# Performance work log

Measured on AMD Instinct MI355X. Metric: run time of the kernel, lower is better.

The kernel has to match this reference:

```python
import jax, jax.numpy as jnp
import numpy as np

N_HEADS = 8
EMBED_DIM = 64  # per-head dim


def setup_inputs() -> dict:
    key = jax.random.key(0)
    k1, k2, k3 = jax.random.split(key, 3)
    B, S, F = 2, 2048, 512
    x = jax.random.normal(k1, (B, S, F), dtype=jnp.float32)
    W = jax.random.normal(k2, (F, EMBED_DIM * N_HEADS * 3), dtype=jnp.float32) * 0.02
    b = jax.random.normal(k3, (EMBED_DIM * N_HEADS * 3,), dtype=jnp.float32) * 0.02
    return {"x": x, "W": W, "b": b}


def reference(x, W, b):
    B, S, F = x.shape
    H, E = N_HEADS, EMBED_DIM
    emb = x @ W + b                                   # (B, S, E*H*3)
    heads = emb.reshape(B, S, E, H, 3)
    heads = jnp.transpose(heads, (0, 4, 3, 1, 2))     # (B, 3, H, S, E)
    q, k, v = heads[:, 0], heads[:, 1], heads[:, 2]   # each (B, H, S, E)
    qk = jnp.einsum('bhse,bhte->bhst', q, k)          # (B, H, S, S)
    # Original multiplies softmax by `scaling` then divides by it -> exact cancel.
    # Note: no scaling applied BEFORE softmax in the source (faithful).
    attn = jax.nn.softmax(qk, axis=-1)
    out = jnp.einsum('bhst,bhte->bhse', attn, v)      # (B, H, S, E)
    out = jnp.transpose(out, (0, 2, 1, 3)).reshape(B, S, H * E)
    return out
```

## Files before the change

kernel.cpp:

```cpp
#include <hip/hip_runtime.h>


using half4v = __attribute__((ext_vector_type(4))) _Float16;
using half8  = __attribute__((ext_vector_type(8))) _Float16;
using f32x4  = __attribute__((ext_vector_type(4))) float;
using float4v = __attribute__((ext_vector_type(4))) float;
using uint2v = __attribute__((ext_vector_type(2))) unsigned int;
using uint4v = __attribute__((ext_vector_type(4))) unsigned int;

constexpr int BN = 2, HN = 8, SN = 2048, EN = 64, FN = 512;
constexpr size_t T_ELEMS = (size_t)BN * HN * SN * EN;

constexpr size_t WD_BYTES = (size_t)1536 * 512 * 2;
constexpr size_t BPN_OFF  = WD_BYTES;
constexpr size_t X16_OFF  = BPN_OFF + 1536 * 4;
constexpr size_t X16_BYTES = (size_t)4096 * 512 * 2;
constexpr size_t VT_OFF   = X16_OFF + X16_BYTES;
constexpr size_t VT_BYTES = T_ELEMS * 2;
constexpr size_t QKV_OFF  = VT_OFF + VT_BYTES;

__device__ inline unsigned int pack2h(float a, float b) {
  auto h = __builtin_amdgcn_cvt_pkrtz(a, b);
  return __builtin_bit_cast(unsigned int, h);
}

__device__ __forceinline__ void async_copy16(void* lds, const void* g) {
  __builtin_amdgcn_global_load_lds(
      (const __attribute__((address_space(1))) unsigned int*)g,
      (__attribute__((address_space(3))) unsigned int*)lds, 16, 0, 0);
}

__global__ __launch_bounds__(256) void prep_kernel(
    const float* __restrict__ x, const float* __restrict__ W,
    const float* __restrict__ bias, _Float16* __restrict__ x16,
    _Float16* __restrict__ Wd, float* __restrict__ bpn) {
  int t = blockIdx.x * 256 + threadIdx.x;
  const float4v* src = (const float4v*)(x + (size_t)t * 8);
  float4v a = src[0], b = src[1];
  half8 o;
  #pragma unroll
  for (int i = 0; i < 4; ++i) { o[i] = (_Float16)a[i]; o[4 + i] = (_Float16)b[i]; }
  *(half8*)(x16 + (size_t)t * 8) = o;

  if (t < 1536 * 64) {
    int n = t >> 6, cc = t & 63, fb = cc * 8;
    int ch = n >> 6, e = n & 63, c = ch >> 3, h = ch & 7;
    int j = e * 24 + h * 3 + c;
    half8 w;
    #pragma unroll
    for (int i = 0; i < 8; ++i) w[i] = (_Float16)W[(size_t)(fb + i) * 1536 + j];
    *(half8*)(Wd + (size_t)n * 512 + fb) = w;
  }
  if (t < 1536) {
    int ch = t >> 6, e = t & 63, c = ch >> 3, h = ch & 7;
    bpn[t] = bias[e * 24 + h * 3 + c];
  }
}

__global__ __launch_bounds__(256, 2) void proj_kernel(
    const _Float16* __restrict__ x16, const _Float16* __restrict__ Wd,
    const float* __restrict__ bpn, _Float16* __restrict__ qkv,
    _Float16* __restrict__ vt) {
  __shared__ __align__(16) char smem[65536];

  int tid = threadIdx.x;
  int wave = tid >> 6, lane = tid & 63;
  int q16 = lane & 15, g = lane >> 4;
  int wm = wave >> 1, wn = wave & 1;
  int gm_blk = blockIdx.x * 128, gn_blk = blockIdx.y * 128;

  f32x4 acc[4][4] = {};

  auto stage = [&](int c, int ks) {
    char* Ab = smem + c * 16384;
    char* Bb = smem + 32768 + c * 16384;
    int k0 = ks * 64;
    #pragma unroll
    for (int ii = 0; ii < 4; ++ii) {
      int qq = tid + 256 * ii;
      int row = qq >> 3, cc = qq & 7;
      int sc = (cc ^ (row & 7)) * 8;
      async_copy16(Ab + qq * 16, x16 + (size_t)(gm_blk + row) * 512 + k0 + sc);
      async_copy16(Bb + qq * 16, Wd + (size_t)(gn_blk + row) * 512 + k0 + sc);
    }
  };

  auto compute = [&](int c) {
    const char* Ab = smem + c * 16384;
    const char* Bb = smem + 32768 + c * 16384;
    #pragma unroll
    for (int kh = 0; kh < 2; ++kh) {
      half8 af[4], bf[4];
      #pragma unroll
      for (int mt = 0; mt < 4; ++mt) {
        int m = wm * 64 + mt * 16 + q16;
        af[mt] = *(const half8*)(Ab + m * 128 + ((kh * 64 + g * 16) ^ ((m & 7) << 4)));
      }
      #pragma unroll
      for (int nt = 0; nt < 4; ++nt) {
        int n = wn * 64 + nt * 16 + q16;
        bf[nt] = *(const half8*)(Bb + n * 128 + ((kh * 64 + g * 16) ^ ((n & 7) << 4)));
      }
      __builtin_amdgcn_s_setprio(1);
      #pragma unroll
      for (int mt = 0; mt < 4; ++mt)
        #pragma unroll
        for (int nt = 0; nt < 4; ++nt)
          acc[mt][nt] = __builtin_amdgcn_mfma_f32_16x16x32_f16(af[mt], bf[nt], acc[mt][nt], 0, 0, 0);
      __builtin_amdgcn_s_setprio(0);
    }
  };

  stage(0, 0);
  #pragma unroll
  for (int ks = 0; ks < 8; ++ks) {
    int cur = ks & 1;
    __syncthreads();
    if (ks + 1 < 8) {
      stage(cur ^ 1, ks + 1);
      asm volatile("s_waitcnt vmcnt(8)" ::: "memory");
    } else {
      asm volatile("s_waitcnt vmcnt(0)" ::: "memory");
    }
    __syncthreads();
    compute(cur);
  }

  int gn0 = gn_blk + wn * 64;
  int ch = gn0 >> 6, c = ch >> 3, h = ch & 7;
  int gm0 = gm_blk + wm * 64;
  if (c < 2) {
    _Float16* dst = qkv + (size_t)c * T_ELEMS;
    #pragma unroll
    for (int nt = 0; nt < 4; ++nt) {
      int e = nt * 16 + q16;
      float bv = bpn[gn0 + nt * 16 + q16];
      #pragma unroll
      for (int mt = 0; mt < 4; ++mt)
        #pragma unroll
        for (int r = 0; r < 4; ++r) {
          int gm = gm0 + mt * 16 + g * 4 + r;
          int b = gm >> 11, s = gm & 2047;
          dst[((size_t)(b * HN + h) * SN + s) * EN + e] = (_Float16)(acc[mt][nt][r] + bv);
        }
    }
  } else {
    #pragma unroll
    for (int nt = 0; nt < 4; ++nt) {
      int e = nt * 16 + q16;
      float bv = bpn[gn0 + nt * 16 + q16];
      #pragma unroll
      for (int mt = 0; mt < 4; ++mt) {
        int gm = gm0 + mt * 16 + g * 4;
        int b = gm >> 11, s = gm & 2047;
        half4v hv;
        #pragma unroll
        for (int r = 0; r < 4; ++r) hv[r] = (_Float16)(acc[mt][nt][r] + bv);
        *(half4v*)(vt + ((size_t)(b * HN + h) * EN + e) * SN + s) = hv;
      }
    }
  }
}

__global__ __launch_bounds__(256, 2) void attn_kernel(
    const _Float16* __restrict__ q_ws, const _Float16* __restrict__ k_ws,
    const _Float16* __restrict__ vt_ws, float* __restrict__ out) {
  __shared__ __align__(16) char smem[57344];

  int bid = blockIdx.x;
  int lb = (bid & 7) * 64 + (bid >> 3);
  int bh = lb >> 5, qblk = lb & 31;
  int wave = threadIdx.x >> 6, lane = threadIdx.x & 63;
  int q = lane & 15, g = lane >> 4;
  int q0 = qblk * 64 + wave * 16;

  const _Float16* qb  = q_ws  + ((size_t)bh * SN + q0) * EN;
  const _Float16* kb  = k_ws  + (size_t)bh * SN * EN;
  const _Float16* vtb = vt_ws + (size_t)bh * EN * SN;

  half8 qf[2];
  qf[0] = *(const half8*)(qb + (size_t)q * EN + g * 8);
  qf[1] = *(const half8*)(qb + (size_t)q * EN + 32 + g * 8);

  f32x4 o[4] = {};
  float m = -3e38f, l = 0.f;
  unsigned int* pw = (unsigned int*)(smem + 49152 + wave * 2048);

  int sub = lane >> 3;
  int off8 = ((lane & 7) ^ sub) * 8;
  int lin = lane * 16;

  auto stage = [&](int c, int t) {
    char* kbuf = smem + c * 16384;
    char* vbuf = kbuf + 8192;
    int kv = t * 64;
    #pragma unroll
    for (int ii = 0; ii < 2; ++ii) {
      int i = wave * 2 + ii;
      int row = i * 8 + sub;
      async_copy16(kbuf + i * 1024 + lin, kb + (size_t)(kv + row) * EN + off8);
      async_copy16(vbuf + i * 1024 + lin, vtb + (size_t)row * SN + kv + off8);
    }
  };

  int qx = (q & 7) << 4;

  auto compute = [&](int c) {
    const char* kbuf = smem + c * 16384;
    const char* vbuf = kbuf + 8192;
    half8 kf[4][2], vf[4][2];
    #pragma unroll
    for (int kt = 0; kt < 4; ++kt)
      #pragma unroll
      for (int eh = 0; eh < 2; ++eh)
        kf[kt][eh] = *(const half8*)(kbuf + ((((kt * 16 + q) * 128) + eh * 64 + g * 16) ^ qx));
    #pragma unroll
    for (int et = 0; et < 4; ++et)
      #pragma unroll
      for (int kh = 0; kh < 2; ++kh)
        vf[et][kh] = *(const half8*)(vbuf + ((((et * 16 + q) * 128) + kh * 64 + g * 16) ^ qx));

    f32x4 s[4];
    f32x4 z = {};
    __builtin_amdgcn_s_setprio(1);
    #pragma unroll
    for (int kt = 0; kt < 4; ++kt) {
      s[kt] = __builtin_amdgcn_mfma_f32_16x16x32_f16(kf[kt][0], qf[0], z, 0, 0, 0);
      s[kt] = __builtin_amdgcn_mfma_f32_16x16x32_f16(kf[kt][1], qf[1], s[kt], 0, 0, 0);
    }
    __builtin_amdgcn_s_setprio(0);

    float mx = s[0][0];
    #pragma unroll
    for (int kt = 0; kt < 4; ++kt)
      #pragma unroll
      for (int r = 0; r < 4; ++r) mx = fmaxf(mx, s[kt][r]);
    mx = fmaxf(mx, __shfl_xor(mx, 16));
    mx = fmaxf(mx, __shfl_xor(mx, 32));
    if (!__all(mx <= m + 8.f)) {
      float mn = fmaxf(m, mx);
      float scl = __expf(m - mn);
      m = mn;
      l *= scl;
      #pragma unroll
      for (int et = 0; et < 4; ++et)
        #pragma unroll
        for (int r = 0; r < 4; ++r) o[et][r] *= scl;
    }
    float ps = 0.f;
    #pragma unroll
    for (int kt = 0; kt < 4; ++kt) {
      float p0 = __expf(s[kt][0] - m), p1 = __expf(s[kt][1] - m);
      float p2 = __expf(s[kt][2] - m), p3 = __expf(s[kt][3] - m);
      ps += (p0 + p1) + (p2 + p3);
      uint2v wv;
      wv.x = pack2h(p0, p1);
      wv.y = pack2h(p2, p3);
      int w = kt * 8 + 2 * g;
      int phys = (((w >> 2) + q) & 7) * 4 + (w & 3);
      *(uint2v*)&pw[q * 32 + phys] = wv;
    }
    l += ps;
    asm volatile("s_waitcnt lgkmcnt(0)" ::: "memory");
    __builtin_amdgcn_sched_barrier(0);
    half8 pf[2];
    #pragma unroll
    for (int kh = 0; kh < 2; ++kh) {
      int cc = kh * 4 + g;
      uint4v tv = *(const uint4v*)&pw[q * 32 + ((cc + q) & 7) * 4];
      pf[kh] = __builtin_bit_cast(half8, tv);
    }
    __builtin_amdgcn_sched_barrier(0);
    __builtin_amdgcn_s_setprio(1);
    #pragma unroll
    for (int et = 0; et < 4; ++et) {
      o[et] = __builtin_amdgcn_mfma_f32_16x16x32_f16(vf[et][0], pf[0], o[et], 0, 0, 0);
      o[et] = __builtin_amdgcn_mfma_f32_16x16x32_f16(vf[et][1], pf[1], o[et], 0, 0, 0);
    }
    __builtin_amdgcn_s_setprio(0);
  };

  stage(0, 0);
  stage(1, 1);
  for (int t = 0; t < 31; ++t) {
    asm volatile("s_waitcnt vmcnt(4)" ::: "memory");
    __syncthreads();
    if (t + 2 < 32) stage((t + 2) % 3, t + 2);
    compute(t % 3);
  }
  asm volatile("s_waitcnt vmcnt(0)" ::: "memory");
  __syncthreads();
  compute(31 % 3);

  l += __shfl_xor(l, 16);
  l += __shfl_xor(l, 32);
  float rl = 1.f / l;
  int b = bh >> 3, h = bh & 7;
  float* ow = (float*)(smem + wave * 4096);
  #pragma unroll
  for (int et = 0; et < 4; ++et)
    #pragma unroll
    for (int r = 0; r < 4; ++r) {
      int e = et * 16 + g * 4 + r;
      ow[q * 64 + ((e + q * 4) & 63)] = o[et][r] * rl;
    }
  asm volatile("s_waitcnt lgkmcnt(0)" ::: "memory");
  __builtin_amdgcn_sched_barrier(0);
  #pragma unroll
  for (int qr = 0; qr < 16; ++qr) {
    float vvv = ow[qr * 64 + ((lane + qr * 4) & 63)];
    out[((size_t)b * SN + q0 + qr) * 512 + h * 64 + lane] = vvv;
  }
}

extern "C" void kernel_launch(void* const* d_in, const int* in_sizes, int n_in,
                              void* d_out, int out_size, void* d_ws, size_t ws_size,
                              hipStream_t stream) {
  const float* x    = (const float*)d_in[0];
  const float* W    = (const float*)d_in[1];
  const float* bias = (const float*)d_in[2];
  float* out = (float*)d_out;
  char* ws = (char*)d_ws;
  _Float16* Wd  = (_Float16*)(ws);
  float*    bpn = (float*)(ws + BPN_OFF);
  _Float16* x16 = (_Float16*)(ws + X16_OFF);
  _Float16* vt  = (_Float16*)(ws + VT_OFF);
  _Float16* qkv = (_Float16*)(ws + QKV_OFF);

  prep_kernel<<<1024, 256, 0, stream>>>(x, W, bias, x16, Wd, bpn);
  proj_kernel<<<dim3(32, 12), 256, 0, stream>>>(x16, Wd, bpn, qkv, vt);
  attn_kernel<<<512, 256, 0, stream>>>(qkv, qkv + T_ELEMS, vt, out);
}
```

Before: 120.1 us.

## Software-pipeline QK and PV across tiles, use exp2 with prescaled Q, shuffle P

Splits the attention inner step into a QK MFMA stage and a softmax+PV stage, then interleaves them so that the QK of tile t+1 is issued before the PV of tile t. Q is prescaled by log2(e) in the projection epilogue, so the softmax can use exp2f, and the rescale threshold is raised accordingly. The P matrix is now redistributed between lanes with cross-lane shuffles instead of an LDS round trip, which frees the per-wave P scratch area in shared memory. In exchange the kernel carries two score tile sets in registers, waits for all outstanding loads (vmcnt(0)) each step, and issues many shuffles, which may raise register pressure and stall the loads.

```diff
diff --git a/kernel.cpp b/kernel.cpp
--- a/kernel.cpp
+++ b/kernel.cpp
@@ -5,11 +5,11 @@
 using half8  = __attribute__((ext_vector_type(8))) _Float16;
 using f32x4  = __attribute__((ext_vector_type(4))) float;
 using float4v = __attribute__((ext_vector_type(4))) float;
-using uint2v = __attribute__((ext_vector_type(2))) unsigned int;
 using uint4v = __attribute__((ext_vector_type(4))) unsigned int;
 
 constexpr int BN = 2, HN = 8, SN = 2048, EN = 64, FN = 512;
 constexpr size_t T_ELEMS = (size_t)BN * HN * SN * EN;
+constexpr float LOG2E = 1.4426950408889634f;
 
 constexpr size_t WD_BYTES = (size_t)1536 * 512 * 2;
 constexpr size_t BPN_OFF  = WD_BYTES;
@@ -130,6 +130,7 @@
   int ch = gn0 >> 6, c = ch >> 3, h = ch & 7;
   int gm0 = gm_blk + wm * 64;
   if (c < 2) {
+    float qscale = (c == 0) ? LOG2E : 1.f;
     _Float16* dst = qkv + (size_t)c * T_ELEMS;
     #pragma unroll
     for (int nt = 0; nt < 4; ++nt) {
@@ -141,7 +142,7 @@
         for (int r = 0; r < 4; ++r) {
           int gm = gm0 + mt * 16 + g * 4 + r;
           int b = gm >> 11, s = gm & 2047;
-          dst[((size_t)(b * HN + h) * SN + s) * EN + e] = (_Float16)(acc[mt][nt][r] + bv);
+          dst[((size_t)(b * HN + h) * SN + s) * EN + e] = (_Float16)((acc[mt][nt][r] + bv) * qscale);
         }
     }
   } else {
@@ -165,7 +166,7 @@
 __global__ __launch_bounds__(256, 2) void attn_kernel(
     const _Float16* __restrict__ q_ws, const _Float16* __restrict__ k_ws,
     const _Float16* __restrict__ vt_ws, float* __restrict__ out) {
-  __shared__ __align__(16) char smem[57344];
+  __shared__ __align__(16) char smem[49152];
 
   int bid = blockIdx.x;
   int lb = (bid & 7) * 64 + (bid >> 3);
@@ -184,7 +185,6 @@
 
   f32x4 o[4] = {};
   float m = -3e38f, l = 0.f;
-  unsigned int* pw = (unsigned int*)(smem + 49152 + wave * 2048);
 
   int sub = lane >> 3;
   int off8 = ((lane & 7) ^ sub) * 8;
@@ -204,23 +204,18 @@
   };
 
   int qx = (q & 7) << 4;
-
-  auto compute = [&](int c) {
+  int srcA = q + 32 * (g & 1);
+  int srcB = srcA + 16;
+  bool hi = (g >> 1) != 0;
+
+  auto qk_tile = [&](int c, f32x4 (&s)[4]) {
     const char* kbuf = smem + c * 16384;
-    const char* vbuf = kbuf + 8192;
-    half8 kf[4][2], vf[4][2];
+    half8 kf[4][2];
     #pragma unroll
     for (int kt = 0; kt < 4; ++kt)
       #pragma unroll
       for (int eh = 0; eh < 2; ++eh)
         kf[kt][eh] = *(const half8*)(kbuf + ((((kt * 16 + q) * 128) + eh * 64 + g * 16) ^ qx));
-    #pragma unroll
-    for (int et = 0; et < 4; ++et)
-      #pragma unroll
-      for (int kh = 0; kh < 2; ++kh)
-        vf[et][kh] = *(const half8*)(vbuf + ((((et * 16 + q) * 128) + kh * 64 + g * 16) ^ qx));
-
-    f32x4 s[4];
     f32x4 z = {};
     __builtin_amdgcn_s_setprio(1);
     #pragma unroll
@@ -229,6 +224,16 @@
       s[kt] = __builtin_amdgcn_mfma_f32_16x16x32_f16(kf[kt][1], qf[1], s[kt], 0, 0, 0);
     }
     __builtin_amdgcn_s_setprio(0);
+  };
+
+  auto finish_pv = [&](f32x4 (&s)[4], int c) {
+    const char* vbuf = smem + c * 16384 + 8192;
+    half8 vf[4][2];
+    #pragma unroll
+    for (int et = 0; et < 4; ++et)
+      #pragma unroll
+      for (int kh = 0; kh < 2; ++kh)
+        vf[et][kh] = *(const half8*)(vbuf + ((((et * 16 + q) * 128) + kh * 64 + g * 16) ^ qx));
 
     float mx = s[0][0];
     #pragma unroll
@@ -237,9 +242,9 @@
       for (int r = 0; r < 4; ++r) mx = fmaxf(mx, s[kt][r]);
     mx = fmaxf(mx, __shfl_xor(mx, 16));
     mx = fmaxf(mx, __shfl_xor(mx, 32));
-    if (!__all(mx <= m + 8.f)) {
+    if (!__all(mx <= m + 12.f)) {
       float mn = fmaxf(m, mx);
-      float scl = __expf(m - mn);
+      float scl = exp2f(m - mn);
       m = mn;
       l *= scl;
       #pragma unroll
@@ -248,50 +253,73 @@
         for (int r = 0; r < 4; ++r) o[et][r] *= scl;
     }
     float ps = 0.f;
-    #pragma unroll
-    for (int kt = 0; kt < 4; ++kt) {
-      float p0 = __expf(s[kt][0] - m), p1 = __expf(s[kt][1] - m);
-      float p2 = __expf(s[kt][2] - m), p3 = __expf(s[kt][3] - m);
-      ps += (p0 + p1) + (p2 + p3);
-      uint2v wv;
-      wv.x = pack2h(p0, p1);
-      wv.y = pack2h(p2, p3);
-      int w = kt * 8 + 2 * g;
-      int phys = (((w >> 2) + q) & 7) * 4 + (w & 3);
-      *(uint2v*)&pw[q * 32 + phys] = wv;
+    unsigned w00, w01, w10, w11, w20, w21, w30, w31;
+    {
+      float p0, p1, p2, p3;
+      p0 = exp2f(s[0][0] - m); p1 = exp2f(s[0][1] - m); p2 = exp2f(s[0][2] - m); p3 = exp2f(s[0][3] - m);
+      ps += (p0 + p1) + (p2 + p3); w00 = pack2h(p0, p1); w01 = pack2h(p2, p3);
+      p0 = exp2f(s[1][0] - m); p1 = exp2f(s[1][1] - m); p2 = exp2f(s[1][2] - m); p3 = exp2f(s[1][3] - m);
+      ps += (p0 + p1) + (p2 + p3); w10 = pack2h(p0, p1); w11 = pack2h(p2, p3);
+      p0 = exp2f(s[2][0] - m); p1 = exp2f(s[2][1] - m); p2 = exp2f(s[2][2] - m); p3 = exp2f(s[2][3] - m);
+      ps += (p0 + p1) + (p2 + p3); w20 = pack2h(p0, p1); w21 = pack2h(p2, p3);
+      p0 = exp2f(s[3][0] - m); p1 = exp2f(s[3][1] - m); p2 = exp2f(s[3][2] - m); p3 = exp2f(s[3][3] - m);
+      ps += (p0 + p1) + (p2 + p3); w30 = pack2h(p0, p1); w31 = pack2h(p2, p3);
     }
     l += ps;
-    asm volatile("s_waitcnt lgkmcnt(0)" ::: "memory");
-    __builtin_amdgcn_sched_barrier(0);
-    half8 pf[2];
-    #pragma unroll
-    for (int kh = 0; kh < 2; ++kh) {
-      int cc = kh * 4 + g;
-      uint4v tv = *(const uint4v*)&pw[q * 32 + ((cc + q) & 7) * 4];
-      pf[kh] = __builtin_bit_cast(half8, tv);
-    }
-    __builtin_amdgcn_sched_barrier(0);
+    uint4v pv0, pv1;
+    {
+      unsigned xa0 = __shfl(w00, srcA), ya0 = __shfl(w10, srcA);
+      unsigned xa1 = __shfl(w01, srcA), ya1 = __shfl(w11, srcA);
+      unsigned xb0 = __shfl(w00, srcB), yb0 = __shfl(w10, srcB);
+      unsigned xb1 = __shfl(w01, srcB), yb1 = __shfl(w11, srcB);
+      pv0.x = hi ? ya0 : xa0; pv0.y = hi ? ya1 : xa1;
+      pv0.z = hi ? yb0 : xb0; pv0.w = hi ? yb1 : xb1;
+      unsigned za0 = __shfl(w20, srcA), ua0 = __shfl(w30, srcA);
+      unsigned za1 = __shfl(w21, srcA), ua1 = __shfl(w31, srcA);
+      unsigned zb0 = __shfl(w20, srcB), ub0 = __shfl(w30, srcB);
+      unsigned zb1 = __shfl(w21, srcB), ub1 = __shfl(w31, srcB);
+      pv1.x = hi ? ua0 : za0; pv1.y = hi ? ua1 : za1;
+      pv1.z = hi ? ub0 : zb0; pv1.w = hi ? ub1 : zb1;
+    }
+    half8 pf0 = __builtin_bit_cast(half8, pv0);
+    half8 pf1 = __builtin_bit_cast(half8, pv1);
     __builtin_amdgcn_s_setprio(1);
     #pragma unroll
     for (int et = 0; et < 4; ++et) {
-      o[et] = __builtin_amdgcn_mfma_f32_16x16x32_f16(vf[et][0], pf[0], o[et], 0, 0, 0);
-      o[et] = __builtin_amdgcn_mfma_f32_16x16x32_f16(vf[et][1], pf[1], o[et], 0, 0, 0);
+      o[et] = __builtin_amdgcn_mfma_f32_16x16x32_f16(vf[et][0], pf0, o[et], 0, 0, 0);
+      o[et] = __builtin_amdgcn_mfma_f32_16x16x32_f16(vf[et][1], pf1, o[et], 0, 0, 0);
     }
     __builtin_amdgcn_s_setprio(0);
   };
+
+  f32x4 sA[4], sB[4];
 
   stage(0, 0);
   stage(1, 1);
-  for (int t = 0; t < 31; ++t) {
-    asm volatile("s_waitcnt vmcnt(4)" ::: "memory");
+  asm volatile("s_waitcnt vmcnt(4)" ::: "memory");
+  __syncthreads();
+  qk_tile(0, sA);
+
+  for (int t0 = 0; t0 < 30; t0 += 2) {
+    asm volatile("s_waitcnt vmcnt(0)" ::: "memory");
     __syncthreads();
-    if (t + 2 < 32) stage((t + 2) % 3, t + 2);
-    compute(t % 3);
+    stage((t0 + 2) % 3, t0 + 2);
+    qk_tile((t0 + 1) % 3, sB);
+    finish_pv(sA, t0 % 3);
+
+    asm volatile("s_waitcnt vmcnt(0)" ::: "memory");
+    __syncthreads();
+    stage((t0 + 3) % 3, t0 + 3);
+    qk_tile((t0 + 2) % 3, sA);
+    finish_pv(sB, (t0 + 1) % 3);
   }
   asm volatile("s_waitcnt vmcnt(0)" ::: "memory");
   __syncthreads();
-  compute(31 % 3);
-
+  qk_tile(31 % 3, sB);
+  finish_pv(sA, 30 % 3);
+  finish_pv(sB, 31 % 3);
+
+  __syncthreads();
   l += __shfl_xor(l, 16);
   l += __shfl_xor(l, 32);
   float rl = 1.f / l;
```

Result: slower. 134.2 us (+11.7%).

## Widen attention blocks to 8 waves and fold log2e into Q for exp2 softmax

Applied to the files above, without the earlier changes.

Attention blocks now hold 8 waves (128 query rows) and share each staged K/V tile. This halves the global K/V traffic per query row and gives one async copy per thread per tile. Q is pre-scaled by log2(e) in the projection epilogue so the softmax can use exp2f, and the rescale threshold is widened. K/V fragments are now loaded from LDS just before each MFMA pair rather than all at once, to reduce register pressure. A barrier is added before the output staging, which reuses the LDS buffers. The larger block (64KB LDS, 512 threads) limits occupancy per CU, and Q stored in fp16 now carries the extra scale factor.

```diff
diff --git a/kernel.cpp b/kernel.cpp
--- a/kernel.cpp
+++ b/kernel.cpp
@@ -10,6 +10,7 @@
 
 constexpr int BN = 2, HN = 8, SN = 2048, EN = 64, FN = 512;
 constexpr size_t T_ELEMS = (size_t)BN * HN * SN * EN;
+constexpr float LOG2E = 1.4426950408889634f;
 
 constexpr size_t WD_BYTES = (size_t)1536 * 512 * 2;
 constexpr size_t BPN_OFF  = WD_BYTES;
@@ -130,6 +131,7 @@
   int ch = gn0 >> 6, c = ch >> 3, h = ch & 7;
   int gm0 = gm_blk + wm * 64;
   if (c < 2) {
+    float qscale = (c == 0) ? LOG2E : 1.f;
     _Float16* dst = qkv + (size_t)c * T_ELEMS;
     #pragma unroll
     for (int nt = 0; nt < 4; ++nt) {
@@ -141,7 +143,7 @@
         for (int r = 0; r < 4; ++r) {
           int gm = gm0 + mt * 16 + g * 4 + r;
           int b = gm >> 11, s = gm & 2047;
-          dst[((size_t)(b * HN + h) * SN + s) * EN + e] = (_Float16)(acc[mt][nt][r] + bv);
+          dst[((size_t)(b * HN + h) * SN + s) * EN + e] = (_Float16)((acc[mt][nt][r] + bv) * qscale);
         }
     }
   } else {
@@ -162,17 +164,18 @@
   }
 }
 
-__global__ __launch_bounds__(256, 2) void attn_kernel(
+__global__ __launch_bounds__(512, 4) void attn_kernel(
     const _Float16* __restrict__ q_ws, const _Float16* __restrict__ k_ws,
     const _Float16* __restrict__ vt_ws, float* __restrict__ out) {
-  __shared__ __align__(16) char smem[57344];
+  __shared__ __align__(16) char smem[65536];
 
   int bid = blockIdx.x;
-  int lb = (bid & 7) * 64 + (bid >> 3);
-  int bh = lb >> 5, qblk = lb & 31;
-  int wave = threadIdx.x >> 6, lane = threadIdx.x & 63;
+  int lb = (bid & 7) * 32 + (bid >> 3);
+  int bh = lb >> 4, qblk = lb & 15;
+  int tid = threadIdx.x;
+  int wave = tid >> 6, lane = tid & 63;
   int q = lane & 15, g = lane >> 4;
-  int q0 = qblk * 64 + wave * 16;
+  int q0 = qblk * 128 + wave * 16;
 
   const _Float16* qb  = q_ws  + ((size_t)bh * SN + q0) * EN;
   const _Float16* kb  = k_ws  + (size_t)bh * SN * EN;
@@ -186,21 +189,16 @@
   float m = -3e38f, l = 0.f;
   unsigned int* pw = (unsigned int*)(smem + 49152 + wave * 2048);
 
-  int sub = lane >> 3;
-  int off8 = ((lane & 7) ^ sub) * 8;
-  int lin = lane * 16;
+  int srow = tid >> 3;
+  int soff8 = ((tid & 7) ^ (srow & 7)) * 8;
+  int slin = tid * 16;
 
   auto stage = [&](int c, int t) {
     char* kbuf = smem + c * 16384;
     char* vbuf = kbuf + 8192;
     int kv = t * 64;
-    #pragma unroll
-    for (int ii = 0; ii < 2; ++ii) {
-      int i = wave * 2 + ii;
-      int row = i * 8 + sub;
-      async_copy16(kbuf + i * 1024 + lin, kb + (size_t)(kv + row) * EN + off8);
-      async_copy16(vbuf + i * 1024 + lin, vtb + (size_t)row * SN + kv + off8);
-    }
+    async_copy16(kbuf + slin, kb + (size_t)(kv + srow) * EN + soff8);
+    async_copy16(vbuf + slin, vtb + (size_t)srow * SN + kv + soff8);
   };
 
   int qx = (q & 7) << 4;
@@ -208,27 +206,18 @@
   auto compute = [&](int c) {
     const char* kbuf = smem + c * 16384;
     const char* vbuf = kbuf + 8192;
-    half8 kf[4][2], vf[4][2];
-    #pragma unroll
-    for (int kt = 0; kt < 4; ++kt)
-      #pragma unroll
-      for (int eh = 0; eh < 2; ++eh)
-        kf[kt][eh] = *(const half8*)(kbuf + ((((kt * 16 + q) * 128) + eh * 64 + g * 16) ^ qx));
-    #pragma unroll
-    for (int et = 0; et < 4; ++et)
-      #pragma unroll
-      for (int kh = 0; kh < 2; ++kh)
-        vf[et][kh] = *(const half8*)(vbuf + ((((et * 16 + q) * 128) + kh * 64 + g * 16) ^ qx));
 
     f32x4 s[4];
     f32x4 z = {};
-    __builtin_amdgcn_s_setprio(1);
     #pragma unroll
     for (int kt = 0; kt < 4; ++kt) {
-      s[kt] = __builtin_amdgcn_mfma_f32_16x16x32_f16(kf[kt][0], qf[0], z, 0, 0, 0);
-      s[kt] = __builtin_amdgcn_mfma_f32_16x16x32_f16(kf[kt][1], qf[1], s[kt], 0, 0, 0);
-    }
-    __builtin_amdgcn_s_setprio(0);
+      half8 kf0 = *(const half8*)(kbuf + ((((kt * 16 + q) * 128) + g * 16) ^ qx));
+      half8 kf1 = *(const half8*)(kbuf + ((((kt * 16 + q) * 128) + 64 + g * 16) ^ qx));
+      __builtin_amdgcn_s_setprio(1);
+      s[kt] = __builtin_amdgcn_mfma_f32_16x16x32_f16(kf0, qf[0], z, 0, 0, 0);
+      s[kt] = __builtin_amdgcn_mfma_f32_16x16x32_f16(kf1, qf[1], s[kt], 0, 0, 0);
+      __builtin_amdgcn_s_setprio(0);
+    }
 
     float mx = s[0][0];
     #pragma unroll
@@ -237,9 +226,9 @@
       for (int r = 0; r < 4; ++r) mx = fmaxf(mx, s[kt][r]);
     mx = fmaxf(mx, __shfl_xor(mx, 16));
     mx = fmaxf(mx, __shfl_xor(mx, 32));
-    if (!__all(mx <= m + 8.f)) {
+    if (!__all(mx <= m + 12.f)) {
       float mn = fmaxf(m, mx);
-      float scl = __expf(m - mn);
+      float scl = exp2f(m - mn);
       m = mn;
       l *= scl;
       #pragma unroll
@@ -250,8 +239,8 @@
     float ps = 0.f;
     #pragma unroll
     for (int kt = 0; kt < 4; ++kt) {
-      float p0 = __expf(s[kt][0] - m), p1 = __expf(s[kt][1] - m);
-      float p2 = __expf(s[kt][2] - m), p3 = __expf(s[kt][3] - m);
+      float p0 = exp2f(s[kt][0] - m), p1 = exp2f(s[kt][1] - m);
+      float p2 = exp2f(s[kt][2] - m), p3 = exp2f(s[kt][3] - m);
       ps += (p0 + p1) + (p2 + p3);
       uint2v wv;
       wv.x = pack2h(p0, p1);
@@ -271,19 +260,21 @@
       pf[kh] = __builtin_bit_cast(half8, tv);
     }
     __builtin_amdgcn_sched_barrier(0);
-    __builtin_amdgcn_s_setprio(1);
     #pragma unroll
     for (int et = 0; et < 4; ++et) {
-      o[et] = __builtin_amdgcn_mfma_f32_16x16x32_f16(vf[et][0], pf[0], o[et], 0, 0, 0);
-      o[et] = __builtin_amdgcn_mfma_f32_16x16x32_f16(vf[et][1], pf[1], o[et], 0, 0, 0);
-    }
-    __builtin_amdgcn_s_setprio(0);
+      half8 vf0 = *(const half8*)(vbuf + ((((et * 16 + q) * 128) + g * 16) ^ qx));
+      half8 vf1 = *(const half8*)(vbuf + ((((et * 16 + q) * 128) + 64 + g * 16) ^ qx));
+      __builtin_amdgcn_s_setprio(1);
+      o[et] = __builtin_amdgcn_mfma_f32_16x16x32_f16(vf0, pf[0], o[et], 0, 0, 0);
+      o[et] = __builtin_amdgcn_mfma_f32_16x16x32_f16(vf1, pf[1], o[et], 0, 0, 0);
+      __builtin_amdgcn_s_setprio(0);
+    }
   };
 
   stage(0, 0);
   stage(1, 1);
   for (int t = 0; t < 31; ++t) {
-    asm volatile("s_waitcnt vmcnt(4)" ::: "memory");
+    asm volatile("s_waitcnt vmcnt(2)" ::: "memory");
     __syncthreads();
     if (t + 2 < 32) stage((t + 2) % 3, t + 2);
     compute(t % 3);
@@ -292,6 +283,7 @@
   __syncthreads();
   compute(31 % 3);
 
+  __syncthreads();
   l += __shfl_xor(l, 16);
   l += __shfl_xor(l, 32);
   float rl = 1.f / l;
@@ -329,5 +321,5 @@
 
   prep_kernel<<<1024, 256, 0, stream>>>(x, W, bias, x16, Wd, bpn);
   proj_kernel<<<dim3(32, 12), 256, 0, stream>>>(x16, Wd, bpn, qkv, vt);
-  attn_kernel<<<512, 256, 0, stream>>>(qkv, qkv + T_ELEMS, vt, out);
-}
+  attn_kernel<<<256, 512, 0, stream>>>(qkv, qkv + T_ELEMS, vt, out);
+}
```

New measurement: 127.2 us. +5.9%, slower.
